# Kernel tuning notes

Hardware: AMD Instinct MI355X
Metric: run time of the kernel (lower is better)

## Reference

```python
import jax, jax.numpy as jnp
import numpy as np

EPS = 1e-5

def maxpool2(x):
    # 2x2 max pool, stride 2, NCHW
    B, C, H, W = x.shape
    return x.reshape(B, C, H // 2, 2, W // 2, 2).max(axis=(3, 5))

def conv1x1(x, w, b):
    # x: [B,C,H,W], w: [O,C], b: [O]
    return jnp.einsum('bchw,oc->bohw', x, w) + b[None, :, None, None]

def setup_inputs() -> dict:
    key = jax.random.key(0)
    ks = jax.random.split(key, 12)
    B, C, IC, H, W = 8, 256, 128, 128, 128
    s = 0.05
    return {
        'rgb': jax.random.normal(ks[0], (B, C, H, W), jnp.float32),
        'event': jax.random.normal(ks[1], (B, C, H, W), jnp.float32),
        'g_w': jax.random.normal(ks[2], (IC, C), jnp.float32) * s,
        'g_b': jax.random.normal(ks[3], (IC,), jnp.float32) * s,
        'theta_w': jax.random.normal(ks[4], (IC, C), jnp.float32) * s,
        'theta_b': jax.random.normal(ks[5], (IC,), jnp.float32) * s,
        'phi_w': jax.random.normal(ks[6], (IC, C), jnp.float32) * s,
        'phi_b': jax.random.normal(ks[7], (IC,), jnp.float32) * s,
        'W_w': jax.random.normal(ks[8], (C, IC), jnp.float32) * s,
        'W_b': jax.random.normal(ks[9], (C,), jnp.float32) * s,
        'bn_gamma': jax.random.normal(ks[10], (C,), jnp.float32) * s + 1.0,
        'bn_beta': jax.random.normal(ks[11], (C,), jnp.float32) * s,
    }

def reference(rgb, event, g_w, g_b, theta_w, theta_b, phi_w, phi_b, W_w, W_b, bn_gamma, bn_beta):
    B = rgb.shape[0]
    IC = g_w.shape[0]
    # initial shared 2x2 max pool on both modalities
    rgb_p = maxpool2(rgb)      # [B,C,h2,w2]
    ev_p = maxpool2(event)
    h2, w2 = rgb_p.shape[2], rgb_p.shape[3]
    # projections; g and phi have an extra sub_sample pool
    g_x = maxpool2(conv1x1(ev_p, g_w, g_b)).reshape(B, IC, -1)      # [B,IC,Nkv]
    g_x = jnp.swapaxes(g_x, 1, 2)                                    # [B,Nkv,IC]
    theta_x = conv1x1(rgb_p, theta_w, theta_b).reshape(B, IC, -1)    # [B,IC,Nq]
    theta_x = jnp.swapaxes(theta_x, 1, 2)                            # [B,Nq,IC]
    phi_x = maxpool2(conv1x1(ev_p, phi_w, phi_b)).reshape(B, IC, -1) # [B,IC,Nkv]
    # full attention: scores -> softmax -> value matmul
    f = jnp.einsum('bqc,bck->bqk', theta_x, phi_x)                   # [B,Nq,Nkv]
    f_div_C = jax.nn.softmax(f, axis=-1)
    y = jnp.einsum('bqk,bkc->bqc', f_div_C, g_x)                     # [B,Nq,IC]
    y = jnp.swapaxes(y, 1, 2).reshape(B, IC, h2, w2)
    # output 1x1 conv + BatchNorm (training-mode batch stats, biased var)
    W_y = conv1x1(y, W_w, W_b)                                       # [B,C,h2,w2]
    mean = W_y.mean(axis=(0, 2, 3), keepdims=True)
    var = W_y.var(axis=(0, 2, 3), keepdims=True)
    W_y = (W_y - mean) * jax.lax.rsqrt(var + EPS)
    W_y = W_y * bn_gamma[None, :, None, None] + bn_beta[None, :, None, None]
    z = W_y + rgb_p
    z = jnp.repeat(jnp.repeat(z, 2, axis=2), 2, axis=3)
    return z
```

## Files before the change

### kernel.cpp

```cpp
#include <hip/hip_runtime.h>
#include <stdint.h>


typedef unsigned short u16;
typedef short bf16x8 __attribute__((ext_vector_type(8)));
typedef float f32x4 __attribute__((ext_vector_type(4)));

#define MFMA16(a, b, c) __builtin_amdgcn_mfma_f32_16x16x32_bf16(a, b, c, 0, 0, 0)

__device__ __forceinline__ u16 f2bf(float x) {
    union { float f; unsigned int u; } v; v.f = x;
    unsigned int u = v.u;
    unsigned int r = u + 0x7fffu + ((u >> 16) & 1u);
    return (u16)(r >> 16);
}
__device__ __forceinline__ float bf2f(u16 h) {
    union { unsigned int u; float f; } v; v.u = ((unsigned int)h) << 16;
    return v.f;
}

__global__ void wsplit_kernel(const float* __restrict__ tw, const float* __restrict__ pw,
                              const float* __restrict__ gw, const float* __restrict__ ww,
                              u16* __restrict__ planes, float* __restrict__ acc) {
    if (blockIdx.x == 0) {
        acc[threadIdx.x] = 0.0f;
        acc[256 + threadIdx.x] = 0.0f;
    }
    int idx = blockIdx.x * 256 + threadIdx.x;
    int m = idx >> 15, p = idx & 32767;
    const float* src = (m == 0) ? tw : (m == 1) ? pw : (m == 2) ? gw : ww;
    int se;
    if (m < 3) {
        int e = p & 7, lane = (p >> 3) & 63, kc = (p >> 9) & 7, ocb = p >> 12;
        int l16 = lane & 15, quad = lane >> 4;
        se = (ocb * 16 + l16) * 256 + kc * 32 + quad * 8 + e;
    } else {
        se = p;
    }
    float v = src[se];
    u16 h = f2bf(v);
    planes[m * 65536 + p] = h;
    planes[m * 65536 + 32768 + p] = f2bf(v - bf2f(h));
}

__global__ __launch_bounds__(512) void fused_pool_conv_kernel(
    const float* __restrict__ xr, const float* __restrict__ xe,
    const u16* __restrict__ Th, const u16* __restrict__ Tl, const float* __restrict__ tb,
    const u16* __restrict__ Fh, const u16* __restrict__ Fl, const float* __restrict__ fb,
    const u16* __restrict__ Gh, const float* __restrict__ gb,
    u16* __restrict__ th_o, u16* __restrict__ tl_o,
    u16* __restrict__ fh_o, u16* __restrict__ fl_o,
    u16* __restrict__ g_o, u16* __restrict__ pool_hi) {
    __shared__ u16 Ph[64 * 256];
    __shared__ u16 Plo[64 * 256];

    int bx = blockIdx.x;
    bool ev = bx >= 512;
    int bxx = bx & 511;
    int b = bxx >> 6, h2 = bxx & 63;
    int tid = threadIdx.x;
    int lane = tid & 63, quad = lane >> 4, l16 = lane & 15;
    int w = tid >> 6, mhalf = w & 1, nq = w >> 1;

    const float* x = ev ? xe : xr;
    const u16* W1h = ev ? Fh : Th;
    const u16* W1l = ev ? Fl : Tl;
    const float* b1 = ev ? fb : tb;
    u16* o1_hi = ev ? fh_o : th_o;
    u16* o1_lo = ev ? fl_o : tl_o;

    bf16x8 wh[2][2], wl[2][2], wg[2][2];
#pragma unroll
    for (int nt = 0; nt < 2; nt++) {
        long wo = ((long)((nq * 2 + nt) * 8 + 0) * 64 + lane) * 8;
        wh[0][nt] = *(const bf16x8*)&W1h[wo];
        wl[0][nt] = *(const bf16x8*)&W1l[wo];
        if (ev) wg[0][nt] = *(const bf16x8*)&Gh[wo];
    }

    long ibase = (long)b * 256 * 16384 + (long)(2 * h2) * 128;
    int coff = (bx * 37) & 255;
#pragma unroll 8
    for (int i = 0; i < 16; i++) {
        int u = i * 512 + tid;
        int c0 = u >> 5, w4 = u & 31;
        int c = (c0 + coff) & 255;
        const float* p = &x[ibase + (long)c * 16384 + w4 * 4];
        float4 r0 = *(const float4*)p;
        float4 r1 = *(const float4*)(p + 128);
        float p0 = fmaxf(fmaxf(r0.x, r0.y), fmaxf(r1.x, r1.y));
        float p1 = fmaxf(fmaxf(r0.z, r0.w), fmaxf(r1.z, r1.w));
        int row0 = 2 * w4, row1 = row0 + 1;
        int g = c >> 3, e = c & 7;
        u16 h0 = f2bf(p0), l0 = f2bf(p0 - bf2f(h0));
        u16 h1 = f2bf(p1), l1 = f2bf(p1 - bf2f(h1));
        int o0 = row0 * 256 + (((g ^ (row0 & 31)) << 3) | e);
        int o1 = row1 * 256 + (((g ^ (row1 & 31)) << 3) | e);
        Ph[o0] = h0; Plo[o0] = l0;
        Ph[o1] = h1; Plo[o1] = l1;
    }
    __syncthreads();

    f32x4 a1[2][2];
    f32x4 a2[2][2];
#pragma unroll
    for (int mt = 0; mt < 2; mt++)
#pragma unroll
        for (int nt = 0; nt < 2; nt++) {
#pragma unroll
            for (int r = 0; r < 4; r++) a1[mt][nt][r] = 0.0f;
#pragma unroll
            for (int r = 0; r < 4; r++) a2[mt][nt][r] = 0.0f;
        }

#pragma unroll
    for (int kc = 0; kc < 8; kc++) {
        int cur = kc & 1, nxt = cur ^ 1;
        if (kc < 7) {
#pragma unroll
            for (int nt = 0; nt < 2; nt++) {
                long wo = ((long)((nq * 2 + nt) * 8 + (kc + 1)) * 64 + lane) * 8;
                wh[nxt][nt] = *(const bf16x8*)&W1h[wo];
                wl[nxt][nt] = *(const bf16x8*)&W1l[wo];
                if (ev) wg[nxt][nt] = *(const bf16x8*)&Gh[wo];
            }
        }
        bf16x8 ah[2], al[2];
#pragma unroll
        for (int mt = 0; mt < 2; mt++) {
            int arow = mhalf * 32 + mt * 16 + l16;
            int g = kc * 4 + quad;
            int off = arow * 256 + ((g ^ (arow & 31)) << 3);
            ah[mt] = *(const bf16x8*)&Ph[off];
            al[mt] = *(const bf16x8*)&Plo[off];
        }
#pragma unroll
        for (int mt = 0; mt < 2; mt++)
#pragma unroll
            for (int nt = 0; nt < 2; nt++) {
                a1[mt][nt] = MFMA16(ah[mt], wh[cur][nt], a1[mt][nt]);
                a1[mt][nt] = MFMA16(ah[mt], wl[cur][nt], a1[mt][nt]);
                a1[mt][nt] = MFMA16(al[mt], wh[cur][nt], a1[mt][nt]);
                if (ev) a2[mt][nt] = MFMA16(ah[mt], wg[cur][nt], a2[mt][nt]);
            }
    }

    long mbase = (long)b * 4096 + h2 * 64;
#pragma unroll
    for (int mt = 0; mt < 2; mt++)
#pragma unroll
        for (int nt = 0; nt < 2; nt++) {
            int colo = nq * 32 + nt * 16 + l16;
            float bv1 = b1[colo];
            float bv2 = ev ? gb[colo] : 0.0f;
#pragma unroll
            for (int r = 0; r < 4; r++) {
                long row = mbase + mhalf * 32 + mt * 16 + quad * 4 + r;
                long idx = row * 128 + colo;
                float v = a1[mt][nt][r] + bv1;
                u16 h = f2bf(v);
                o1_hi[idx] = h;
                o1_lo[idx] = f2bf(v - bf2f(h));
                if (ev) g_o[idx] = f2bf(a2[mt][nt][r] + bv2);
            }
        }

    if (!ev) {
#pragma unroll 4
        for (int i = 0; i < 16; i++) {
            int r = i * 4 + (tid >> 7);
            int c = (tid & 127) * 2;
            int g = c >> 3;
            ushort2 hh = *(const ushort2*)&Ph[r * 256 + (((g ^ (r & 31)) << 3) | (c & 7))];
            *(ushort2*)&pool_hi[(mbase + r) * 256 + c] = hh;
        }
    }
}

__global__ __launch_bounds__(256) void pool_mid_kernel(
    const u16* __restrict__ fhi, const u16* __restrict__ flo,
    u16* __restrict__ khi, u16* __restrict__ klo,
    const u16* __restrict__ gsrc, u16* __restrict__ vt) {
    __shared__ u16 t[64][65];
    int bX = blockIdx.x;
    int tid = threadIdx.x;
    if (bX < 512) {
        int idx = bX * 256 + tid;
        int c8 = (idx & 15) * 8;
        int kv = (idx >> 4) & 1023;
        int b = idx >> 14;
        int h4 = kv >> 5, w4 = kv & 31;
        long p00 = ((long)b * 4096 + (2 * h4) * 64 + 2 * w4) * 128 + c8;
        bf16x8 h0 = *(const bf16x8*)&fhi[p00];
        bf16x8 h1 = *(const bf16x8*)&fhi[p00 + 128];
        bf16x8 h2 = *(const bf16x8*)&fhi[p00 + 8192];
        bf16x8 h3 = *(const bf16x8*)&fhi[p00 + 8320];
        bf16x8 l0 = *(const bf16x8*)&flo[p00];
        bf16x8 l1 = *(const bf16x8*)&flo[p00 + 128];
        bf16x8 l2 = *(const bf16x8*)&flo[p00 + 8192];
        bf16x8 l3 = *(const bf16x8*)&flo[p00 + 8320];
        bf16x8 oh, ol;
#pragma unroll
        for (int e = 0; e < 8; e++) {
            float v = fmaxf(fmaxf(bf2f((u16)h0[e]) + bf2f((u16)l0[e]),
                                  bf2f((u16)h1[e]) + bf2f((u16)l1[e])),
                            fmaxf(bf2f((u16)h2[e]) + bf2f((u16)l2[e]),
                                  bf2f((u16)h3[e]) + bf2f((u16)l3[e])));
            u16 h = f2bf(v);
            oh[e] = (short)h;
            ol[e] = (short)f2bf(v - bf2f(h));
        }
        long oi = ((long)b * 1024 + kv) * 128 + c8;
        *(bf16x8*)&khi[oi] = oh;
        *(bf16x8*)&klo[oi] = ol;
    } else {
        int bx = bX - 512;
        int ct = bx & 1, kvt = (bx >> 1) & 15, b = bx >> 5;
#pragma unroll 4
        for (int i = 0; i < 16; i++) {
            int idx = i * 256 + tid;
            int kv_l = idx >> 6, c_l = idx & 63;
            int kv = kvt * 64 + kv_l;
            int h4 = kv >> 5, w4 = kv & 31;
            long p00 = ((long)b * 4096 + (2 * h4) * 64 + 2 * w4) * 128 + ct * 64 + c_l;
            float v = fmaxf(fmaxf(bf2f(gsrc[p00]), bf2f(gsrc[p00 + 128])),
                            fmaxf(bf2f(gsrc[p00 + 8192]), bf2f(gsrc[p00 + 8192 + 128])));
            t[c_l][kv_l] = f2bf(v);
        }
        __syncthreads();
        long ob = ((long)b * 128 + ct * 64) * 1024 + kvt * 64;
#pragma unroll 4
        for (int i = 0; i < 16; i++) {
            int idx = i * 256 + tid;
            int c_l = idx >> 6, kv_l = idx & 63;
            vt[ob + (long)c_l * 1024 + kv_l] = t[c_l][kv_l];
        }
    }
}

__global__ __launch_bounds__(512, 4) void attn_kernel(
    const u16* __restrict__ th, const u16* __restrict__ tl,
    const u16* __restrict__ khi, const u16* __restrict__ klo,
    const u16* __restrict__ vt, u16* __restrict__ y) {
    __shared__ u16 Kh[2][32][136];
    __shared__ u16 Kl[2][32][136];
    __shared__ u16 Vt[2][128][40];
    __shared__ u16 Pl[8][16][40];

    int bx = blockIdx.x;
    int b = bx & 7, qt = bx >> 3;
    int tid = threadIdx.x;
    int w = tid >> 6, g = w >> 2, wsub = w & 3;
    int lane = tid & 63, quad = lane >> 4, l16 = lane & 15;
    int qbase = qt * 64 + wsub * 16;

    int krow = (tid >> 4) & 31, kko = (tid & 15) * 8;
    int vrow = (tid >> 2) & 127, vko = (tid & 3) * 8;
    long kb0 = ((long)b * 1024 + krow) * 128 + kko;
    long vb0 = ((long)b * 128 + vrow) * 1024 + vko;
    uint4 rkh0, rkh1, rkl0, rkl1, rv0, rv1;

#define STAGE_LOAD(IT) do {                                   \
        long k0 = kb0 + (long)(IT) * 4096;                    \
        rkh0 = *(const uint4*)&khi[k0];                       \
        rkl0 = *(const uint4*)&klo[k0];                       \
        rkh1 = *(const uint4*)&khi[k0 + 65536];               \
        rkl1 = *(const uint4*)&klo[k0 + 65536];               \
        long v0 = vb0 + (IT) * 32;                            \
        rv0 = *(const uint4*)&vt[v0];                         \
        rv1 = *(const uint4*)&vt[v0 + 512];                   \
    } while (0)

#define STAGE_WRITE() do {                                    \
        *(uint4*)&Kh[0][krow][kko] = rkh0;                    \
        *(uint4*)&Kl[0][krow][kko] = rkl0;                    \
        *(uint4*)&Kh[1][krow][kko] = rkh1;                    \
        *(uint4*)&Kl[1][krow][kko] = rkl1;                    \
        *(uint4*)&Vt[0][vrow][vko] = rv0;                     \
        *(uint4*)&Vt[1][vrow][vko] = rv1;                     \
    } while (0)

    bf16x8 qh[4], ql[4];
    long tb = ((long)b * 4096 + qbase + l16) * 128;
#pragma unroll
    for (int kc = 0; kc < 4; kc++) {
        qh[kc] = *(const bf16x8*)&th[tb + kc * 32 + quad * 8];
        ql[kc] = *(const bf16x8*)&tl[tb + kc * 32 + quad * 8];
    }

    f32x4 o[8];
#pragma unroll
    for (int t2 = 0; t2 < 8; t2++)
#pragma unroll
        for (int r = 0; r < 4; r++) o[t2][r] = 0.0f;
    float lp[4] = {0.0f, 0.0f, 0.0f, 0.0f};

    STAGE_LOAD(0);
    STAGE_WRITE();
    __syncthreads();
    STAGE_LOAD(1);

#pragma unroll 1
    for (int it = 0; it < 16; it++) {
        f32x4 s[2];
#pragma unroll
        for (int nt = 0; nt < 2; nt++)
#pragma unroll
            for (int r = 0; r < 4; r++) s[nt][r] = 0.0f;
#pragma unroll
        for (int kc = 0; kc < 4; kc++) {
#pragma unroll
            for (int nt = 0; nt < 2; nt++) {
                bf16x8 bh = *(const bf16x8*)&Kh[g][nt * 16 + l16][kc * 32 + quad * 8];
                bf16x8 bl = *(const bf16x8*)&Kl[g][nt * 16 + l16][kc * 32 + quad * 8];
                s[nt] = MFMA16(qh[kc], bh, s[nt]);
                s[nt] = MFMA16(qh[kc], bl, s[nt]);
                s[nt] = MFMA16(ql[kc], bh, s[nt]);
            }
        }

#pragma unroll
        for (int nt = 0; nt < 2; nt++)
#pragma unroll
            for (int r = 0; r < 4; r++) {
                float p = __expf(s[nt][r]);
                lp[r] += p;
                Pl[w][quad * 4 + r][nt * 16 + l16] = f2bf(p);
            }

        bf16x8 pa = *(const bf16x8*)&Pl[w][l16][quad * 8];
#pragma unroll
        for (int t2 = 0; t2 < 8; t2++) {
            bf16x8 vb = *(const bf16x8*)&Vt[g][t2 * 16 + l16][quad * 8];
            o[t2] = MFMA16(pa, vb, o[t2]);
        }

        __syncthreads();
        if (it < 15) {
            STAGE_WRITE();
            __syncthreads();
            if (it < 14) STAGE_LOAD(it + 2);
        }
    }

#pragma unroll
    for (int r = 0; r < 4; r++)
#pragma unroll
        for (int off = 1; off < 16; off <<= 1) lp[r] += __shfl_xor(lp[r], off);

    __syncthreads();
    float* Ob = (float*)&Kh[0][0][0];
    float* Lb = (float*)&Vt[0][0][0];
    if (g == 1) {
#pragma unroll
        for (int t2 = 0; t2 < 8; t2++)
#pragma unroll
            for (int r = 0; r < 4; r++)
                Ob[(wsub * 16 + quad * 4 + r) * 132 + t2 * 16 + l16] = o[t2][r];
        if (l16 == 0)
#pragma unroll
            for (int r = 0; r < 4; r++) Lb[wsub * 16 + quad * 4 + r] = lp[r];
    }
    __syncthreads();
    if (g == 0) {
#pragma unroll
        for (int r = 0; r < 4; r++) {
            int lrow = wsub * 16 + quad * 4 + r;
            float inv = 1.0f / (lp[r] + Lb[lrow]);
            long row = (long)b * 4096 + qbase + quad * 4 + r;
#pragma unroll
            for (int t2 = 0; t2 < 8; t2++) {
                float ov = o[t2][r] + Ob[lrow * 132 + t2 * 16 + l16];
                y[row * 128 + t2 * 16 + l16] = f2bf(ov * inv);
            }
        }
    }
#undef STAGE_LOAD
#undef STAGE_WRITE
}

__global__ __launch_bounds__(256) void wconv_kernel(
    const u16* __restrict__ A, const u16* __restrict__ Wh,
    const float* __restrict__ bias, float* __restrict__ out_f,
    float* __restrict__ acc_g) {
    __shared__ float red[4][2][256];
    int tid = threadIdx.x;
    int wave = tid >> 6, lane = tid & 63, quad = lane >> 4, l16 = lane & 15;
    long mbase = (long)blockIdx.x * 64 + wave * 16;

    f32x4 acc[16];
#pragma unroll
    for (int nt = 0; nt < 16; nt++)
#pragma unroll
        for (int r = 0; r < 4; r++) acc[nt][r] = 0.0f;

#pragma unroll
    for (int kc = 0; kc < 4; kc++) {
        bf16x8 ah = *(const bf16x8*)&A[(mbase + l16) * 128 + kc * 32 + quad * 8];
#pragma unroll
        for (int nt = 0; nt < 16; nt++) {
            bf16x8 bh = *(const bf16x8*)&Wh[(long)(nt * 16 + l16) * 128 + kc * 32 + quad * 8];
            acc[nt] = MFMA16(ah, bh, acc[nt]);
        }
    }

#pragma unroll
    for (int nt = 0; nt < 16; nt++) {
        int colo = nt * 16 + l16;
        float bv = bias[colo];
        float vs = 0.0f, vq = 0.0f;
#pragma unroll
        for (int r = 0; r < 4; r++) {
            long row = mbase + quad * 4 + r;
            float v = acc[nt][r] + bv;
            out_f[row * 256 + colo] = v;
            vs += v;
            vq += v * v;
        }
        vs += __shfl_xor(vs, 16); vs += __shfl_xor(vs, 32);
        vq += __shfl_xor(vq, 16); vq += __shfl_xor(vq, 32);
        if (quad == 0) {
            red[wave][0][colo] = vs;
            red[wave][1][colo] = vq;
        }
    }
    __syncthreads();
    if (tid < 256) {
        int c = tid;
        float s = red[0][0][c] + red[1][0][c] + red[2][0][c] + red[3][0][c];
        float q = red[0][1][c] + red[1][1][c] + red[2][1][c] + red[3][1][c];
        atomicAdd(&acc_g[c], s);
        atomicAdd(&acc_g[256 + c], q);
    }
}

__global__ __launch_bounds__(256) void final_kernel(
    const float* __restrict__ wy, const u16* __restrict__ rgbhi,
    const float* __restrict__ acc, const float* __restrict__ gamma,
    const float* __restrict__ beta, float* __restrict__ out) {
    __shared__ float z[16][257];
    int bx = blockIdx.x;
    int wt = bx & 3, h2 = (bx >> 2) & 63, b = bx >> 8;
    int c = threadIdx.x;

    float mean = acc[c] * (1.0f / 32768.0f);
    float var = acc[256 + c] * (1.0f / 32768.0f) - mean * mean;
    float rstd = rsqrtf(var + 1e-5f);
    float gm = gamma[c] * rstd;
    float bt = beta[c] - mean * gm;

    long pbase = (long)b * 4096 + h2 * 64 + wt * 16;
#pragma unroll 4
    for (int i = 0; i < 16; i++) {
        long pi = (pbase + i) * 256 + c;
        z[i][c] = wy[pi] * gm + bt + bf2f(rgbhi[pi]);
    }
    __syncthreads();
    int tid = threadIdx.x;
#pragma unroll 4
    for (int pass = 0; pass < 64; pass++) {
        int cc = pass * 4 + (tid >> 6);
        int r = (tid >> 5) & 1, wc = tid & 31;
        float v = z[wc >> 1][cc];
        out[(((long)b * 256 + cc) * 128 + 2 * h2 + r) * 128 + wt * 32 + wc] = v;
    }
}

extern "C" void kernel_launch(void* const* d_in, const int* in_sizes, int n_in,
                              void* d_out, int out_size, void* d_ws, size_t ws_size,
                              hipStream_t stream) {
    const float* rgb     = (const float*)d_in[0];
    const float* event_  = (const float*)d_in[1];
    const float* g_w     = (const float*)d_in[2];
    const float* g_b     = (const float*)d_in[3];
    const float* theta_w = (const float*)d_in[4];
    const float* theta_b = (const float*)d_in[5];
    const float* phi_w   = (const float*)d_in[6];
    const float* phi_b   = (const float*)d_in[7];
    const float* W_w     = (const float*)d_in[8];
    const float* W_b     = (const float*)d_in[9];
    const float* gamma   = (const float*)d_in[10];
    const float* beta    = (const float*)d_in[11];

    char* ws = (char*)d_ws;
    u16* rgbpt_hi = (u16*)(ws + 0);
    u16* theta_hi = (u16*)(ws + 16777216);
    u16* theta_lo = (u16*)(ws + 25165824);
    u16* phiF_hi  = (u16*)(ws + 33554432);
    u16* phiF_lo  = (u16*)(ws + 41943040);
    u16* g_full   = (u16*)(ws + 50331648);
    u16* phiK_hi  = (u16*)(ws + 58720256);
    u16* phiK_lo  = (u16*)(ws + 60817408);
    u16* gVt      = (u16*)(ws + 62914560);
    u16* y        = (u16*)(ws + 65011712);
    float* Wy     = (float*)(ws + 73400320);
    u16* wplanes  = (u16*)(ws + 106954752);
    float* acc    = (float*)(ws + 107479040);

    wsplit_kernel<<<512, 256, 0, stream>>>(theta_w, phi_w, g_w, W_w, wplanes, acc);

    fused_pool_conv_kernel<<<1024, 512, 0, stream>>>(
        rgb, event_,
        wplanes + 0, wplanes + 32768, theta_b,
        wplanes + 65536, wplanes + 98304, phi_b,
        wplanes + 131072, g_b,
        theta_hi, theta_lo, phiF_hi, phiF_lo, g_full, rgbpt_hi);

    pool_mid_kernel<<<768, 256, 0, stream>>>(phiF_hi, phiF_lo, phiK_hi, phiK_lo,
                                             g_full, gVt);

    attn_kernel<<<512, 512, 0, stream>>>(theta_hi, theta_lo, phiK_hi, phiK_lo, gVt, y);

    wconv_kernel<<<512, 256, 0, stream>>>(y, wplanes + 196608, W_b, Wy, acc);

    final_kernel<<<2048, 256, 0, stream>>>(Wy, rgbpt_hi, acc, gamma, beta, (float*)d_out);
}
```

Baseline: 462.6 us.

## Register-pack pooled channels and write LDS as 16-byte vectors with new swizzle

The pooling stage is restructured so that each thread owns 16 consecutive channels for one pair of output columns. Its global loads are software-pipelined in two register buffers, and the bf16 hi/lo values are packed into bf16x8 vectors that go to LDS as 16-byte stores. This replaces the scattered 2-byte LDS stores, and the XOR swizzle changes to use the row index halved so the writes and the MFMA reads stay consistent. Launch bounds now request four blocks per CU, which raises register pressure from the larger live set and may cause spills.

```diff
diff --git a/kernel.cpp b/kernel.cpp
--- a/kernel.cpp
+++ b/kernel.cpp
@@ -43,7 +43,7 @@
     planes[m * 65536 + 32768 + p] = f2bf(v - bf2f(h));
 }
 
-__global__ __launch_bounds__(512) void fused_pool_conv_kernel(
+__global__ __launch_bounds__(512, 4) void fused_pool_conv_kernel(
     const float* __restrict__ xr, const float* __restrict__ xe,
     const u16* __restrict__ Th, const u16* __restrict__ Tl, const float* __restrict__ tb,
     const u16* __restrict__ Fh, const u16* __restrict__ Fl, const float* __restrict__ fb,
@@ -69,6 +69,62 @@
     u16* o1_hi = ev ? fh_o : th_o;
     u16* o1_lo = ev ? fl_o : tl_o;
 
+    int w4 = tid & 31;
+    int cg = tid >> 5;
+    const float* px = x + (long)b * 256 * 16384 + (long)(2 * h2) * 128
+                        + (long)(cg * 16) * 16384 + w4 * 4;
+
+    bf16x8 h0[2], l0[2], h1[2], l1[2];
+
+#define LOADB(R0, R1, J0)                                            \
+    do {                                                             \
+        _Pragma("unroll")                                            \
+        for (int j = 0; j < 4; j++) {                                \
+            R0[j] = *(const float4*)(px + (long)(J0 + j) * 16384);   \
+            R1[j] = *(const float4*)(px + (long)(J0 + j) * 16384 + 128); \
+        }                                                            \
+    } while (0)
+
+#define PROCB(R0, R1, J0)                                            \
+    do {                                                             \
+        _Pragma("unroll")                                            \
+        for (int j = 0; j < 4; j++) {                                \
+            float p0 = fmaxf(fmaxf(R0[j].x, R0[j].y), fmaxf(R1[j].x, R1[j].y)); \
+            float p1 = fmaxf(fmaxf(R0[j].z, R0[j].w), fmaxf(R1[j].z, R1[j].w)); \
+            int jj = J0 + j, gi = jj >> 3, e = jj & 7;               \
+            u16 a0 = f2bf(p0);                                       \
+            h0[gi][e] = (short)a0; l0[gi][e] = (short)f2bf(p0 - bf2f(a0)); \
+            u16 a1 = f2bf(p1);                                       \
+            h1[gi][e] = (short)a1; l1[gi][e] = (short)f2bf(p1 - bf2f(a1)); \
+        }                                                            \
+    } while (0)
+
+    {
+        float4 A0[4], A1[4], B0[4], B1[4];
+        LOADB(A0, A1, 0);
+        LOADB(B0, B1, 4);
+        PROCB(A0, A1, 0);
+        LOADB(A0, A1, 8);
+        PROCB(B0, B1, 4);
+        LOADB(B0, B1, 12);
+        PROCB(A0, A1, 8);
+        PROCB(B0, B1, 12);
+    }
+#undef LOADB
+#undef PROCB
+
+    {
+        int row0 = 2 * w4, row1 = row0 + 1;
+#pragma unroll
+        for (int gi = 0; gi < 2; gi++) {
+            int pg = ((cg * 2 + gi) ^ w4) & 31;
+            *(bf16x8*)&Ph[row0 * 256 + pg * 8] = h0[gi];
+            *(bf16x8*)&Ph[row1 * 256 + pg * 8] = h1[gi];
+            *(bf16x8*)&Plo[row0 * 256 + pg * 8] = l0[gi];
+            *(bf16x8*)&Plo[row1 * 256 + pg * 8] = l1[gi];
+        }
+    }
+
     bf16x8 wh[2][2], wl[2][2], wg[2][2];
 #pragma unroll
     for (int nt = 0; nt < 2; nt++) {
@@ -76,28 +132,6 @@
         wh[0][nt] = *(const bf16x8*)&W1h[wo];
         wl[0][nt] = *(const bf16x8*)&W1l[wo];
         if (ev) wg[0][nt] = *(const bf16x8*)&Gh[wo];
-    }
-
-    long ibase = (long)b * 256 * 16384 + (long)(2 * h2) * 128;
-    int coff = (bx * 37) & 255;
-#pragma unroll 8
-    for (int i = 0; i < 16; i++) {
-        int u = i * 512 + tid;
-        int c0 = u >> 5, w4 = u & 31;
-        int c = (c0 + coff) & 255;
-        const float* p = &x[ibase + (long)c * 16384 + w4 * 4];
-        float4 r0 = *(const float4*)p;
-        float4 r1 = *(const float4*)(p + 128);
-        float p0 = fmaxf(fmaxf(r0.x, r0.y), fmaxf(r1.x, r1.y));
-        float p1 = fmaxf(fmaxf(r0.z, r0.w), fmaxf(r1.z, r1.w));
-        int row0 = 2 * w4, row1 = row0 + 1;
-        int g = c >> 3, e = c & 7;
-        u16 h0 = f2bf(p0), l0 = f2bf(p0 - bf2f(h0));
-        u16 h1 = f2bf(p1), l1 = f2bf(p1 - bf2f(h1));
-        int o0 = row0 * 256 + (((g ^ (row0 & 31)) << 3) | e);
-        int o1 = row1 * 256 + (((g ^ (row1 & 31)) << 3) | e);
-        Ph[o0] = h0; Plo[o0] = l0;
-        Ph[o1] = h1; Plo[o1] = l1;
     }
     __syncthreads();
 
@@ -129,8 +163,7 @@
 #pragma unroll
         for (int mt = 0; mt < 2; mt++) {
             int arow = mhalf * 32 + mt * 16 + l16;
-            int g = kc * 4 + quad;
-            int off = arow * 256 + ((g ^ (arow & 31)) << 3);
+            int off = arow * 256 + ((((kc * 4 + quad) ^ ((arow >> 1) & 31)) & 31) << 3);
             ah[mt] = *(const bf16x8*)&Ph[off];
             al[mt] = *(const bf16x8*)&Plo[off];
         }
@@ -170,8 +203,8 @@
         for (int i = 0; i < 16; i++) {
             int r = i * 4 + (tid >> 7);
             int c = (tid & 127) * 2;
-            int g = c >> 3;
-            ushort2 hh = *(const ushort2*)&Ph[r * 256 + (((g ^ (r & 31)) << 3) | (c & 7))];
+            ushort2 hh = *(const ushort2*)&Ph[r * 256
+                + ((((c >> 3) ^ ((r >> 1) & 31)) & 31) << 3) + (c & 7)];
             *(ushort2*)&pool_hi[(mbase + r) * 256 + c] = hh;
         }
     }
```

Result: no change. 468.0 us (+1.2%).

## Split pooling into separate coalesced kernel writing bf16 hi/lo planes

Applied to the files above, without the earlier changes.

Moves the 2x2 max-pool and bf16 hi/lo split out of the fused conv kernel into a standalone kernel that reads each channel plane contiguously and writes pooled bf16 planes to workspace. The conv kernel then loads these planes and transposes them into its swizzled shared-memory layout. The intent is to replace the strided per-channel global reads with coalesced streaming reads. The cost is an extra kernel launch and an extra write and read of the pooled intermediates through global memory.

```diff
diff --git a/kernel.cpp b/kernel.cpp
--- a/kernel.cpp
+++ b/kernel.cpp
@@ -43,8 +43,45 @@
     planes[m * 65536 + 32768 + p] = f2bf(v - bf2f(h));
 }
 
-__global__ __launch_bounds__(512) void fused_pool_conv_kernel(
+__global__ __launch_bounds__(256) void pool_split_kernel(
     const float* __restrict__ xr, const float* __restrict__ xe,
+    u16* __restrict__ rh, u16* __restrict__ rl,
+    u16* __restrict__ eh, u16* __restrict__ el) {
+    long q = blockIdx.x;
+    int tid = threadIdx.x;
+    const float* pr = xr + q * 16384;
+    const float* pe = xe + q * 16384;
+    long ob = q * 4096;
+#pragma unroll
+    for (int i = 0; i < 8; i++) {
+        int u = i * 256 + tid;
+        int h2 = u >> 5, w4 = u & 31;
+        int so = h2 * 256 + w4 * 4;
+        float4 a0 = *(const float4*)&pr[so];
+        float4 a1 = *(const float4*)&pr[so + 128];
+        float4 b0 = *(const float4*)&pe[so];
+        float4 b1 = *(const float4*)&pe[so + 128];
+        float rp0 = fmaxf(fmaxf(a0.x, a0.y), fmaxf(a1.x, a1.y));
+        float rp1 = fmaxf(fmaxf(a0.z, a0.w), fmaxf(a1.z, a1.w));
+        float ep0 = fmaxf(fmaxf(b0.x, b0.y), fmaxf(b1.x, b1.y));
+        float ep1 = fmaxf(fmaxf(b0.z, b0.w), fmaxf(b1.z, b1.w));
+        long oo = ob + h2 * 64 + 2 * w4;
+        u16 h;
+        ushort2 hh, ll;
+        h = f2bf(rp0); hh.x = h; ll.x = f2bf(rp0 - bf2f(h));
+        h = f2bf(rp1); hh.y = h; ll.y = f2bf(rp1 - bf2f(h));
+        *(ushort2*)&rh[oo] = hh;
+        *(ushort2*)&rl[oo] = ll;
+        h = f2bf(ep0); hh.x = h; ll.x = f2bf(ep0 - bf2f(h));
+        h = f2bf(ep1); hh.y = h; ll.y = f2bf(ep1 - bf2f(h));
+        *(ushort2*)&eh[oo] = hh;
+        *(ushort2*)&el[oo] = ll;
+    }
+}
+
+__global__ __launch_bounds__(512) void conv_kernel(
+    const u16* __restrict__ rhp, const u16* __restrict__ rlp,
+    const u16* __restrict__ ehp, const u16* __restrict__ elp,
     const u16* __restrict__ Th, const u16* __restrict__ Tl, const float* __restrict__ tb,
     const u16* __restrict__ Fh, const u16* __restrict__ Fl, const float* __restrict__ fb,
     const u16* __restrict__ Gh, const float* __restrict__ gb,
@@ -62,13 +99,30 @@
     int lane = tid & 63, quad = lane >> 4, l16 = lane & 15;
     int w = tid >> 6, mhalf = w & 1, nq = w >> 1;
 
-    const float* x = ev ? xe : xr;
     const u16* W1h = ev ? Fh : Th;
     const u16* W1l = ev ? Fl : Tl;
     const float* b1 = ev ? fb : tb;
     u16* o1_hi = ev ? fh_o : th_o;
     u16* o1_lo = ev ? fl_o : tl_o;
 
+    {
+        int c = tid >> 1, pl = tid & 1;
+        const u16* srcp = pl ? (ev ? elp : rlp) : (ev ? ehp : rhp);
+        u16* dst = pl ? Plo : Ph;
+        long base = ((long)b * 256 + c) * 4096 + (long)h2 * 64;
+        int cg = c >> 3, ce = c & 7;
+        bf16x8 v[8];
+#pragma unroll
+        for (int k = 0; k < 8; k++) v[k] = *(const bf16x8*)&srcp[base + k * 8];
+#pragma unroll
+        for (int k = 0; k < 8; k++)
+#pragma unroll
+            for (int e = 0; e < 8; e++) {
+                int row = k * 8 + e;
+                dst[row * 256 + (((cg ^ (row & 31)) << 3) | ce)] = (u16)v[k][e];
+            }
+    }
+
     bf16x8 wh[2][2], wl[2][2], wg[2][2];
 #pragma unroll
     for (int nt = 0; nt < 2; nt++) {
@@ -77,28 +131,6 @@
         wl[0][nt] = *(const bf16x8*)&W1l[wo];
         if (ev) wg[0][nt] = *(const bf16x8*)&Gh[wo];
     }
-
-    long ibase = (long)b * 256 * 16384 + (long)(2 * h2) * 128;
-    int coff = (bx * 37) & 255;
-#pragma unroll 8
-    for (int i = 0; i < 16; i++) {
-        int u = i * 512 + tid;
-        int c0 = u >> 5, w4 = u & 31;
-        int c = (c0 + coff) & 255;
-        const float* p = &x[ibase + (long)c * 16384 + w4 * 4];
-        float4 r0 = *(const float4*)p;
-        float4 r1 = *(const float4*)(p + 128);
-        float p0 = fmaxf(fmaxf(r0.x, r0.y), fmaxf(r1.x, r1.y));
-        float p1 = fmaxf(fmaxf(r0.z, r0.w), fmaxf(r1.z, r1.w));
-        int row0 = 2 * w4, row1 = row0 + 1;
-        int g = c >> 3, e = c & 7;
-        u16 h0 = f2bf(p0), l0 = f2bf(p0 - bf2f(h0));
-        u16 h1 = f2bf(p1), l1 = f2bf(p1 - bf2f(h1));
-        int o0 = row0 * 256 + (((g ^ (row0 & 31)) << 3) | e);
-        int o1 = row1 * 256 + (((g ^ (row1 & 31)) << 3) | e);
-        Ph[o0] = h0; Plo[o0] = l0;
-        Ph[o1] = h1; Plo[o1] = l1;
-    }
     __syncthreads();
 
     f32x4 a1[2][2];
@@ -129,8 +161,7 @@
 #pragma unroll
         for (int mt = 0; mt < 2; mt++) {
             int arow = mhalf * 32 + mt * 16 + l16;
-            int g = kc * 4 + quad;
-            int off = arow * 256 + ((g ^ (arow & 31)) << 3);
+            int off = arow * 256 + ((((kc * 4 + quad) ^ (arow & 31)) & 31) << 3);
             ah[mt] = *(const bf16x8*)&Ph[off];
             al[mt] = *(const bf16x8*)&Plo[off];
         }
@@ -170,8 +201,8 @@
         for (int i = 0; i < 16; i++) {
             int r = i * 4 + (tid >> 7);
             int c = (tid & 127) * 2;
-            int g = c >> 3;
-            ushort2 hh = *(const ushort2*)&Ph[r * 256 + (((g ^ (r & 31)) << 3) | (c & 7))];
+            ushort2 hh = *(const ushort2*)&Ph[r * 256
+                + ((((c >> 3) ^ (r & 31)) & 31) << 3) + (c & 7)];
             *(ushort2*)&pool_hi[(mbase + r) * 256 + c] = hh;
         }
     }
@@ -483,28 +514,35 @@
     const float* beta    = (const float*)d_in[11];
 
     char* ws = (char*)d_ws;
-    u16* rgbpt_hi = (u16*)(ws + 0);
-    u16* theta_hi = (u16*)(ws + 16777216);
-    u16* theta_lo = (u16*)(ws + 25165824);
-    u16* phiF_hi  = (u16*)(ws + 33554432);
-    u16* phiF_lo  = (u16*)(ws + 41943040);
-    u16* g_full   = (u16*)(ws + 50331648);
-    u16* phiK_hi  = (u16*)(ws + 58720256);
-    u16* phiK_lo  = (u16*)(ws + 60817408);
-    u16* gVt      = (u16*)(ws + 62914560);
-    u16* y        = (u16*)(ws + 65011712);
-    float* Wy     = (float*)(ws + 73400320);
-    u16* wplanes  = (u16*)(ws + 106954752);
-    float* acc    = (float*)(ws + 107479040);
+    u16* rgbpt    = (u16*)(ws + 0);
+    u16* rgb_hi   = (u16*)(ws + 16777216);
+    u16* rgb_lo   = (u16*)(ws + 33554432);
+    u16* ev_hi    = (u16*)(ws + 50331648);
+    u16* ev_lo    = (u16*)(ws + 67108864);
+    u16* theta_hi = (u16*)(ws + 83886080);
+    u16* theta_lo = (u16*)(ws + 92274688);
+    u16* phiF_hi  = (u16*)(ws + 100663296);
+    u16* phiF_lo  = (u16*)(ws + 109051904);
+    u16* g_full   = (u16*)(ws + 117440512);
+    u16* phiK_hi  = (u16*)(ws + 125829120);
+    u16* phiK_lo  = (u16*)(ws + 127926272);
+    u16* gVt      = (u16*)(ws + 130023424);
+    u16* y        = (u16*)(ws + 132120576);
+    float* Wy     = (float*)(ws + 140509184);
+    u16* wplanes  = (u16*)(ws + 174063616);
+    float* acc    = (float*)(ws + 174587904);
 
     wsplit_kernel<<<512, 256, 0, stream>>>(theta_w, phi_w, g_w, W_w, wplanes, acc);
 
-    fused_pool_conv_kernel<<<1024, 512, 0, stream>>>(
-        rgb, event_,
+    pool_split_kernel<<<2048, 256, 0, stream>>>(rgb, event_, rgb_hi, rgb_lo,
+                                                ev_hi, ev_lo);
+
+    conv_kernel<<<1024, 512, 0, stream>>>(
+        rgb_hi, rgb_lo, ev_hi, ev_lo,
         wplanes + 0, wplanes + 32768, theta_b,
         wplanes + 65536, wplanes + 98304, phi_b,
         wplanes + 131072, g_b,
-        theta_hi, theta_lo, phiF_hi, phiF_lo, g_full, rgbpt_hi);
+        theta_hi, theta_lo, phiF_hi, phiF_lo, g_full, rgbpt);
 
     pool_mid_kernel<<<768, 256, 0, stream>>>(phiF_hi, phiF_lo, phiK_hi, phiK_lo,
                                              g_full, gVt);
@@ -513,5 +551,5 @@
 
     wconv_kernel<<<512, 256, 0, stream>>>(y, wplanes + 196608, W_b, Wy, acc);
 
-    final_kernel<<<2048, 256, 0, stream>>>(Wy, rgbpt_hi, acc, gamma, beta, (float*)d_out);
-}
+    final_kernel<<<2048, 256, 0, stream>>>(Wy, rgbpt, acc, gamma, beta, (float*)d_out);
+}
```

New measurement: 503.0 us. 1.09x slower.
